# Kernel tuning notes

Hardware: AMD Instinct MI355X
Metric: run time of the kernel (lower is better)

## Reference

```python
import jax, jax.numpy as jnp
import numpy as np
import math

EMB = 64
NEG_INF = -1e30

def _layernorm(x, g, b, eps=1e-5):
    mu = jnp.mean(x, axis=-1, keepdims=True)
    var = jnp.mean((x - mu) ** 2, axis=-1, keepdims=True)
    return (x - mu) * jax.lax.rsqrt(var + eps) * g + b

def setup_inputs() -> dict:
    key = jax.random.key(0)
    ks = jax.random.split(key, 8)
    b, t, n, d = 16, 12, 307, EMB
    s = 1.0 / math.sqrt(d)
    inp = {
        'x': jax.random.normal(ks[0], (b, t, n, d), dtype=jnp.float32),
        'stg': jax.random.uniform(ks[1], (b, n, t, n), dtype=jnp.float32),
        'topk': 3,
        'q_w': jax.random.normal(ks[2], (d, d), dtype=jnp.float32) * s,
        'q_b': jnp.zeros((d,), jnp.float32),
        'k_w': jax.random.normal(ks[3], (d, d), dtype=jnp.float32) * s,
        'k_b': jnp.zeros((d,), jnp.float32),
        'ln_g': jnp.ones((d,), jnp.float32),
        'ln_b': jnp.zeros((d,), jnp.float32),
        'ffn_ln_g': jnp.ones((d,), jnp.float32),
        'ffn_ln_b': jnp.zeros((d,), jnp.float32),
        'fc1_w': jax.random.normal(ks[4], (4 * d, d), dtype=jnp.float32) * s,
        'fc1_b': jnp.zeros((4 * d,), jnp.float32),
        'fc2_w': jax.random.normal(ks[5], (d, 4 * d), dtype=jnp.float32) * (0.5 * s),
        'fc2_b': jnp.zeros((d,), jnp.float32),
    }
    return inp

def reference(x, stg, topk, q_w, q_b, k_w, k_b, ln_g, ln_b, ffn_ln_g, ffn_ln_b, fc1_w, fc1_b, fc2_w, fc2_b):
    b, t, n, d = x.shape
    scale = 1.0 / math.sqrt(d)
    x_ = _layernorm(x, ln_g, ln_b)           # [b,t,n,d]
    y_ = x_[:, -1]                            # [b,n,d] last timestep
    q = y_ @ q_w.T + q_b                      # [b,n,d]
    k = x_ @ k_w.T + k_b                      # [b,t,n,d]
    dg = jnp.einsum('bnd,btmd->bntm', q, k) * scale
    sag = jax.nn.sigmoid(dg) * stg * scale    # gated scores [b,n,t,n]
    sag = sag.reshape(b, n, t * n)
    if topk > 0:
        kk = topk * n if topk < 5 else topk   # mirrors torch's self.topk *= n
        top_values, _ = jax.lax.top_k(sag, kk)
        thr = top_values[..., -1:]
        sag = jnp.where(sag > thr, sag, NEG_INF)  # strict >, as in torch code
    sag = jax.nn.softmax(sag, axis=-1).reshape(b, n, t, n)  # dropout in eval mode = identity
    o = jnp.einsum('bntm,btmd->bnd', sag, x_)
    h = o + y_
    # FFN: pre-norm residual MLP (LayerNorm -> Linear(d,4d) -> ReLU -> Linear(4d,d) + residual)
    z = _layernorm(h, ffn_ln_g, ffn_ln_b)
    z = jax.nn.relu(z @ fc1_w.T + fc1_b) @ fc2_w.T + fc2_b
    return h + z
```

## Files before the change

kernel.cpp:

```cpp
#include <hip/hip_runtime.h>

typedef __bf16 bf16x8 __attribute__((ext_vector_type(8)));
typedef float  f32x4  __attribute__((ext_vector_type(4)));
typedef unsigned short u16x8 __attribute__((ext_vector_type(8)));
typedef unsigned short u16x4 __attribute__((ext_vector_type(4)));

constexpr int BB    = 16;
constexpr int TT    = 12;
constexpr int NN    = 307;
constexpr int TN    = TT * NN;
constexpr int ROWSX = BB * TT * NN;
constexpr int ROWSH = BB * NN;
constexpr int SST1  = 3712;
constexpr int SSTR  = 3840;
constexpr int HPS   = ROWSH * 64;
constexpr int KQ    = 928;
constexpr float SCALE = 0.125f;

__device__ __forceinline__ float wred_sum(float v) {
#pragma unroll
    for (int m = 32; m > 0; m >>= 1) v += __shfl_xor(v, m, 64);
    return v;
}

__global__ void fold_k(const float* __restrict__ qw, const float* __restrict__ qb,
                       const float* __restrict__ kw, const float* __restrict__ kb,
                       float* __restrict__ M, float* __restrict__ b2,
                       float* __restrict__ vv, float* __restrict__ cc) {
    int e = blockIdx.x, d = threadIdx.x;
    float acc = 0.f;
    for (int dp = 0; dp < 64; ++dp) acc += qw[dp * 64 + e] * kw[dp * 64 + d];
    M[e * 64 + d] = acc;
    float vp = wred_sum(qw[d * 64 + e] * kb[d]);
    if (d == 0) vv[e] = vp;
    if (e == 0) {
        float b = 0.f;
        for (int dp = 0; dp < 64; ++dp) b += qb[dp] * kw[dp * 64 + d];
        b2[d] = b;
        float cp = wred_sum(qb[d] * kb[d]);
        if (d == 0) *cc = cp;
    }
}

__global__ void wconv_k(const float* __restrict__ fc1w, const float* __restrict__ fc2w,
                        __bf16* __restrict__ fc1b16, __bf16* __restrict__ fc2b16) {
    int i = blockIdx.x * 256 + threadIdx.x;
    if (i < 16384) fc1b16[i] = (__bf16)fc1w[i];
    else fc2b16[i - 16384] = (__bf16)fc2w[i - 16384];
}

__global__ __launch_bounds__(256) void lnt_k(const float* __restrict__ x,
                                             const float* __restrict__ g,
                                             const float* __restrict__ b,
                                             __bf16* __restrict__ xnb,
                                             __bf16* __restrict__ xnT,
                                             float* __restrict__ y32) {
    __shared__ unsigned short tile[64][65];
    int bb = blockIdx.y, j0 = blockIdx.x * 64, t = threadIdx.x;
    int w = t >> 6, lane = t & 63;
    float gg = g[lane], bbv = b[lane];
    unsigned short* dst = (unsigned short*)xnT;
#pragma unroll 4
    for (int i = 0; i < 16; ++i) {
        int jr = w * 16 + i;
        int j = j0 + jr;
        bool valid = (j < TN);
        float val = valid ? x[((size_t)bb * TN + j) * 64 + lane] : 0.f;
        float mu  = wred_sum(val) * (1.f / 64.f);
        float dv  = val - mu;
        float var = wred_sum(dv * dv) * (1.f / 64.f);
        float xv  = dv * rsqrtf(var + 1e-5f) * gg + bbv;
        if (valid) {
            __bf16 xb = (__bf16)xv;
            xnb[((size_t)bb * TN + j) * 64 + lane] = xb;
            tile[jr][lane] = *(unsigned short*)&xb;
            if (j >= 11 * NN) y32[((size_t)bb * NN + (j - 11 * NN)) * 64 + lane] = xv;
        } else {
            tile[jr][lane] = 0;
        }
    }
    __syncthreads();
#pragma unroll
    for (int i = 0; i < 16; ++i) {
        int f = t + 256 * i, d = f >> 6, jj = f & 63;
        dst[((size_t)bb * 64 + d) * SSTR + j0 + jj] = tile[jj][d];
    }
}

__global__ __launch_bounds__(256) void qt_k(const float* __restrict__ y32,
                                            const float* __restrict__ M,
                                            const float* __restrict__ b2,
                                            const float* __restrict__ vv,
                                            const float* __restrict__ ccp,
                                            __bf16* __restrict__ qtb,
                                            float* __restrict__ cq) {
    int w = threadIdx.x >> 6, l = threadIdx.x & 63;
    int rr = blockIdx.x * 4 + w;
    if (rr >= ROWSH) return;
    float y = y32[rr * 64 + l];
    float acc = b2[l];
#pragma unroll
    for (int e = 0; e < 64; ++e) acc += __shfl(y, e, 64) * M[e * 64 + l];
    qtb[(size_t)rr * 64 + l] = (__bf16)acc;
    float cp = wred_sum(y * vv[l]);
    if (l == 0) cq[rr] = cp + *ccp;
}

__global__ __launch_bounds__(256) void score_k(const __bf16* __restrict__ qtb,
                                               const float* __restrict__ cq,
                                               const __bf16* __restrict__ xnb,
                                               const float* __restrict__ stg,
                                               __bf16* __restrict__ sag) {
    __shared__ unsigned short wb[64 * 144];
    int bb = blockIdx.z, n0 = blockIdx.y * 64, j0 = blockIdx.x * 128;
    int t = threadIdx.x;
    int w = t >> 6, lane = t & 63;
    int m16 = lane & 15, q4 = lane >> 4;

    bf16x8 a[2][2];
#pragma unroll
    for (int jj = 0; jj < 2; ++jj) {
        const bf16x8* ap = (const bf16x8*)(xnb + ((size_t)bb * TN + j0 + (w * 2 + jj) * 16 + m16) * 64);
        a[jj][0] = ap[q4];
        a[jj][1] = ap[q4 + 4];
    }

    f32x4 acc[2][4];
#pragma unroll
    for (int nt = 0; nt < 4; ++nt) {
        const bf16x8* bp = (const bf16x8*)(qtb + ((size_t)bb * NN + n0 + nt * 16 + m16) * 64);
        bf16x8 b0 = bp[q4], b1 = bp[q4 + 4];
#pragma unroll
        for (int jj = 0; jj < 2; ++jj) {
            f32x4 c = {0.f, 0.f, 0.f, 0.f};
            c = __builtin_amdgcn_mfma_f32_16x16x32_bf16(a[jj][0], b0, c, 0, 0, 0);
            c = __builtin_amdgcn_mfma_f32_16x16x32_bf16(a[jj][1], b1, c, 0, 0, 0);
            acc[jj][nt] = c;
        }
    }

    const float* stgb = stg + (size_t)bb * NN * TN;
#pragma unroll
    for (int nt = 0; nt < 4; ++nt) {
        int n = n0 + nt * 16 + m16;
        float cnv = (n < NN) ? cq[bb * NN + n] : 0.f;
        const float* srow = stgb + (size_t)min(n, NN - 1) * TN;
#pragma unroll
        for (int jj = 0; jj < 2; ++jj) {
            int jb = j0 + (w * 2 + jj) * 16 + q4 * 4;
            float4 sv = {0.f, 0.f, 0.f, 0.f};
            if (jb < TN) sv = *(const float4*)(srow + jb);
            u16x4 hw;
            float svv[4] = {sv.x, sv.y, sv.z, sv.w};
#pragma unroll
            for (int r = 0; r < 4; ++r) {
                float dg = (acc[jj][nt][r] + cnv) * SCALE;
                float s  = 1.f / (1.f + __expf(-dg));
                float wv = (jb + r < TN) ? s * svv[r] * SCALE : 0.f;
                __bf16 wb16 = (__bf16)wv;
                hw[r] = *(unsigned short*)&wb16;
            }
            *(u16x4*)&wb[(nt * 16 + m16) * 144 + (w * 2 + jj) * 16 + q4 * 4] = hw;
        }
    }
    __syncthreads();

#pragma unroll
    for (int i = 0; i < 4; ++i) {
        int chunk = t + i * 256;
        int row = chunk >> 4, c8 = (chunk & 15) * 8;
        int n = n0 + row;
        if (n < NN) {
            u16x8 v = *(const u16x8*)&wb[row * 144 + c8];
            *(u16x8*)((unsigned short*)sag + (size_t)(bb * NN + n) * SST1 + j0 + c8) = v;
        }
    }
}

__global__ __launch_bounds__(256) void smax_k(__bf16* __restrict__ sagB,
                                              const int* __restrict__ topk_p,
                                              float* __restrict__ rsum) {
    int t = threadIdx.x;
    int wid = t >> 6, lane = t & 63;
    int row = blockIdx.x * 4 + wid;
    if (row >= ROWSH) return;

    int topkv = *topk_p;
    bool selAll = (topkv <= 0);
    int kk = 0;
    if (!selAll) {
        kk = (topkv < 5) ? topkv * NN : topkv;
        if (kk > TN) kk = TN;
    }

    u16x8* src = (u16x8*)((unsigned short*)sagB + (size_t)row * SST1);
    u16x8 va[8];
#pragma unroll
    for (int ci = 0; ci < 8; ++ci) {
        int c = lane + (ci << 6);
        u16x8 v = {0, 0, 0, 0, 0, 0, 0, 0};
        if (c < 464) v = src[c];
        va[ci] = v;
    }
    int vmb = 0;
#pragma unroll
    for (int ci = 0; ci < 8; ++ci)
#pragma unroll
        for (int e = 0; e < 8; ++e) vmb = max(vmb, (int)va[ci][e]);
#pragma unroll
    for (int m = 32; m > 0; m >>= 1) vmb = max(vmb, __shfl_xor(vmb, m, 64));
    float vmax = __uint_as_float(((unsigned)vmb) << 16);

    unsigned thrb = 0;
    if (!selAll) {
        unsigned lo = 0, hi = (unsigned)vmb;
        while (lo < hi) {
            unsigned mid = (lo + hi) >> 1;
            int cnt = 0;
#pragma unroll
            for (int ci = 0; ci < 8; ++ci)
#pragma unroll
                for (int e = 0; e < 8; ++e)
                    cnt += (int)__popcll(__ballot((unsigned)va[ci][e] > mid));
            if (cnt < kk) hi = mid; else lo = mid + 1;
        }
        thrb = lo;
    }

    float local = 0.f;
#pragma unroll
    for (int ci = 0; ci < 8; ++ci) {
        int c = lane + (ci << 6);
        int nvv = (c < 460) ? 8 : ((c == 460) ? 4 : 0);
#pragma unroll
        for (int e = 0; e < 8; ++e) {
            unsigned u = va[ci][e];
            bool sel = selAll ? (e < nvv) : (u > thrb);
            float ev = sel ? __expf(__uint_as_float(u << 16) - vmax) : 0.f;
            local += ev;
            __bf16 eb = (__bf16)ev;
            va[ci][e] = *(unsigned short*)&eb;
        }
    }
    local = wred_sum(local);
    bool uni = !(local > 0.f);
    if (lane == 0) rsum[row] = uni ? (float)TN : local;

    if (uni) {
        __bf16 one = (__bf16)1.f, zero = (__bf16)0.f;
#pragma unroll
        for (int ci = 0; ci < 8; ++ci) {
            int c = lane + (ci << 6);
            if (c < 464) {
                int nvv = (c < 460) ? 8 : ((c == 460) ? 4 : 0);
                bf16x8 o;
#pragma unroll
                for (int e = 0; e < 8; ++e) o[e] = (e < nvv) ? one : zero;
                *(bf16x8*)&src[c] = o;
            }
        }
    } else {
#pragma unroll
        for (int ci = 0; ci < 8; ++ci) {
            int c = lane + (ci << 6);
            if (c < 464) src[c] = va[ci];
        }
    }
}

__global__ __launch_bounds__(256) void pv_k(const __bf16* __restrict__ sagB,
                                            const __bf16* __restrict__ xnT,
                                            const float* __restrict__ y32,
                                            const float* __restrict__ rsum,
                                            float* __restrict__ hp) {
    int bb = blockIdx.z, kq = blockIdx.y, n0 = blockIdx.x * 16;
    int wid = threadIdx.x >> 6, lane = threadIdx.x & 63;
    int m16 = lane & 15, q4 = lane >> 4;

    int arow = min(n0 + m16, NN - 1);
    const __bf16* ab  = sagB + (size_t)(bb * NN + arow) * SST1 + kq * KQ + q4 * 8;
    const __bf16* bbp = xnT + ((size_t)bb * 64 + wid * 16 + m16) * SSTR + kq * KQ + q4 * 8;

    f32x4 acc0 = {0.f, 0.f, 0.f, 0.f}, acc1 = {0.f, 0.f, 0.f, 0.f};
#pragma unroll 4
    for (int ks = 0; ks < 29; ++ks) {
        bf16x8 a = *(const bf16x8*)(ab + ks * 32);
        bf16x8 b = *(const bf16x8*)(bbp + ks * 32);
        if (ks & 1) acc1 = __builtin_amdgcn_mfma_f32_16x16x32_bf16(a, b, acc1, 0, 0, 0);
        else        acc0 = __builtin_amdgcn_mfma_f32_16x16x32_bf16(a, b, acc0, 0, 0, 0);
    }
#pragma unroll
    for (int r = 0; r < 4; ++r) {
        int n = n0 + q4 * 4 + r;
        if (n < NN) {
            size_t o = (size_t)(bb * NN + n) * 64 + wid * 16 + m16;
            float inv = 1.f / rsum[bb * NN + n];
            float v = (acc0[r] + acc1[r]) * inv;
            if (kq == 0) v += y32[o];
            hp[(size_t)kq * HPS + o] = v;
        }
    }
}

__global__ __launch_bounds__(256) void ffn_k(const float* __restrict__ hp,
                                             const float* __restrict__ g,
                                             const float* __restrict__ bln,
                                             const __bf16* __restrict__ fc1b16,
                                             const float* __restrict__ fc1b,
                                             const __bf16* __restrict__ fc2b16,
                                             const float* __restrict__ fc2b,
                                             float* __restrict__ out) {
    __shared__ __bf16 zb[16 * 68];
    __shared__ __bf16 ab[16 * 264];
    int t = threadIdx.x, r0 = blockIdx.x * 16;
    int wid = t >> 6, lane = t & 63;
    int m16 = lane & 15, q4 = lane >> 4;

#pragma unroll
    for (int q = 0; q < 4; ++q) {
        int rl = wid * 4 + q;
        size_t i = (size_t)(r0 + rl) * 64 + lane;
        float val = hp[i] + hp[HPS + i] + hp[2 * HPS + i] + hp[3 * HPS + i];
        float mu  = wred_sum(val) * (1.f / 64.f);
        float dv  = val - mu;
        float var = wred_sum(dv * dv) * (1.f / 64.f);
        zb[rl * 68 + lane] = (__bf16)(dv * rsqrtf(var + 1e-5f) * g[lane] + bln[lane]);
    }
    __syncthreads();

    bf16x8 a0 = *(const bf16x8*)&zb[m16 * 68 + q4 * 8];
    bf16x8 a1 = *(const bf16x8*)&zb[m16 * 68 + 32 + q4 * 8];
#pragma unroll
    for (int jt2 = 0; jt2 < 4; ++jt2) {
        int j0t = (wid * 4 + jt2) * 16;
        const __bf16* bp = fc1b16 + (size_t)(j0t + m16) * 64 + q4 * 8;
        f32x4 c = {0.f, 0.f, 0.f, 0.f};
        c = __builtin_amdgcn_mfma_f32_16x16x32_bf16(a0, *(const bf16x8*)bp, c, 0, 0, 0);
        c = __builtin_amdgcn_mfma_f32_16x16x32_bf16(a1, *(const bf16x8*)(bp + 32), c, 0, 0, 0);
        int j = j0t + m16;
        float bias = fc1b[j];
#pragma unroll
        for (int r = 0; r < 4; ++r)
            ab[(q4 * 4 + r) * 264 + j] = (__bf16)fmaxf(c[r] + bias, 0.f);
    }
    __syncthreads();

    f32x4 c2a = {0.f, 0.f, 0.f, 0.f}, c2b = {0.f, 0.f, 0.f, 0.f};
    const __bf16* b2p = fc2b16 + (size_t)(wid * 16 + m16) * 256 + q4 * 8;
#pragma unroll
    for (int k8 = 0; k8 < 8; k8 += 2) {
        bf16x8 aa0 = *(const bf16x8*)&ab[m16 * 264 + k8 * 32 + q4 * 8];
        bf16x8 aa1 = *(const bf16x8*)&ab[m16 * 264 + (k8 + 1) * 32 + q4 * 8];
        c2a = __builtin_amdgcn_mfma_f32_16x16x32_bf16(aa0, *(const bf16x8*)(b2p + k8 * 32), c2a, 0, 0, 0);
        c2b = __builtin_amdgcn_mfma_f32_16x16x32_bf16(aa1, *(const bf16x8*)(b2p + (k8 + 1) * 32), c2b, 0, 0, 0);
    }
    int d = wid * 16 + m16;
    float bias2 = fc2b[d];
#pragma unroll
    for (int r = 0; r < 4; ++r) {
        size_t row = (size_t)(r0 + q4 * 4 + r);
        size_t o = row * 64 + d;
        float hsum = hp[o] + hp[HPS + o] + hp[2 * HPS + o] + hp[3 * HPS + o];
        out[o] = hsum + c2a[r] + c2b[r] + bias2;
    }
}

extern "C" void kernel_launch(void* const* d_in, const int* in_sizes, int n_in,
                              void* d_out, int out_size, void* d_ws, size_t ws_size,
                              hipStream_t stream) {
    const float* x    = (const float*)d_in[0];
    const float* stg  = (const float*)d_in[1];
    const int*   topk = (const int*)d_in[2];
    const float* qw   = (const float*)d_in[3];
    const float* qb   = (const float*)d_in[4];
    const float* kw   = (const float*)d_in[5];
    const float* kb   = (const float*)d_in[6];
    const float* lng  = (const float*)d_in[7];
    const float* lnb  = (const float*)d_in[8];
    const float* flng = (const float*)d_in[9];
    const float* flnb = (const float*)d_in[10];
    const float* fc1w = (const float*)d_in[11];
    const float* fc1b = (const float*)d_in[12];
    const float* fc2w = (const float*)d_in[13];
    const float* fc2b = (const float*)d_in[14];
    float* out = (float*)d_out;

    float* ws = (float*)d_ws;
    __bf16* xnb = (__bf16*)ws;
    float* p1   = ws + 1886208;
    __bf16* xnT = (__bf16*)p1;
    float* p2   = p1 + 1966080;
    __bf16* qtb = (__bf16*)p2;
    float* y32  = p2 + 157696;
    float* cq   = y32 + 314368;
    float* M    = cq + 4928;
    float* b2   = M + 4096;
    float* vv   = b2 + 64;
    float* cc   = vv + 64;
    __bf16* fc1b16 = (__bf16*)(cc + 16);
    __bf16* fc2b16 = (__bf16*)((float*)fc1b16 + 8192);
    __bf16* sag = (__bf16*)((float*)fc2b16 + 8192);
    float* hp   = (float*)sag + 9116672;
    float* rsum = hp + 4 * HPS;

    fold_k<<<64, 64, 0, stream>>>(qw, qb, kw, kb, M, b2, vv, cc);
    wconv_k<<<128, 256, 0, stream>>>(fc1w, fc2w, fc1b16, fc2b16);
    lnt_k<<<dim3(58, BB), 256, 0, stream>>>(x, lng, lnb, xnb, xnT, y32);
    qt_k<<<(ROWSH + 3) / 4, 256, 0, stream>>>(y32, M, b2, vv, cc, qtb, cq);
    score_k<<<dim3((TN + 127) / 128, (NN + 63) / 64, BB), 256, 0, stream>>>(qtb, cq, xnb, stg, sag);
    smax_k<<<(ROWSH + 3) / 4, 256, 0, stream>>>(sag, topk, rsum);
    pv_k<<<dim3((NN + 15) / 16, 4, BB), 256, 0, stream>>>(sag, xnT, y32, rsum, hp);
    ffn_k<<<ROWSH / 16, 256, 0, stream>>>(hp, flng, flnb, fc1b16, fc1b, fc2b16, fc2b, out);
}
```

Before: 266.4 us.

## Split layernorm and transpose into separate kernels; prefetch stg loads in score kernel

The fused layernorm-plus-transpose kernel becomes two kernels. One does a row-parallel layernorm with one wave per row across many more blocks. The other transposes the bf16 normalized data through shared memory. In the score kernel the stg gate values and cq loads are issued before the MFMA work to hide global latency, launch bounds request 4 blocks per CU, and the LDS row stride changes from 144 to 152. The split adds a kernel launch and an extra read of xnb in exchange for more parallelism in the layernorm.

After: 256.5 us. -3.7%, faster.

```diff
diff --git a/kernel.cpp b/kernel.cpp
--- a/kernel.cpp
+++ b/kernel.cpp
@@ -15,6 +15,7 @@
 constexpr int SSTR  = 3840;
 constexpr int HPS   = ROWSH * 64;
 constexpr int KQ    = 928;
+constexpr int WBS   = 152;
 constexpr float SCALE = 0.125f;
 
 __device__ __forceinline__ float wred_sum(float v) {
@@ -49,35 +50,38 @@
     else fc2b16[i - 16384] = (__bf16)fc2w[i - 16384];
 }
 
-__global__ __launch_bounds__(256) void lnt_k(const float* __restrict__ x,
-                                             const float* __restrict__ g,
-                                             const float* __restrict__ b,
-                                             __bf16* __restrict__ xnb,
-                                             __bf16* __restrict__ xnT,
-                                             float* __restrict__ y32) {
+__global__ __launch_bounds__(256) void ln_k(const float* __restrict__ x,
+                                            const float* __restrict__ g,
+                                            const float* __restrict__ b,
+                                            __bf16* __restrict__ xnb,
+                                            float* __restrict__ y32) {
+    int w = threadIdx.x >> 6, l = threadIdx.x & 63;
+    int r = blockIdx.x * 4 + w;
+    if (r >= ROWSX) return;
+    float val = x[r * 64 + l];
+    float mu  = wred_sum(val) * (1.f / 64.f);
+    float dv  = val - mu;
+    float var = wred_sum(dv * dv) * (1.f / 64.f);
+    float xv  = dv * rsqrtf(var + 1e-5f) * g[l] + b[l];
+    xnb[(size_t)r * 64 + l] = (__bf16)xv;
+    int t = (r / NN) % TT;
+    if (t == TT - 1) {
+        int bbv = r / (NN * TT), n = r % NN;
+        y32[(bbv * NN + n) * 64 + l] = xv;
+    }
+}
+
+__global__ __launch_bounds__(256) void t_k(const __bf16* __restrict__ xnb,
+                                           __bf16* __restrict__ xnT) {
     __shared__ unsigned short tile[64][65];
     int bb = blockIdx.y, j0 = blockIdx.x * 64, t = threadIdx.x;
-    int w = t >> 6, lane = t & 63;
-    float gg = g[lane], bbv = b[lane];
+    const unsigned short* src = (const unsigned short*)xnb;
     unsigned short* dst = (unsigned short*)xnT;
-#pragma unroll 4
+#pragma unroll
     for (int i = 0; i < 16; ++i) {
-        int jr = w * 16 + i;
+        int f = t + 256 * i, jr = f >> 6, dc = f & 63;
         int j = j0 + jr;
-        bool valid = (j < TN);
-        float val = valid ? x[((size_t)bb * TN + j) * 64 + lane] : 0.f;
-        float mu  = wred_sum(val) * (1.f / 64.f);
-        float dv  = val - mu;
-        float var = wred_sum(dv * dv) * (1.f / 64.f);
-        float xv  = dv * rsqrtf(var + 1e-5f) * gg + bbv;
-        if (valid) {
-            __bf16 xb = (__bf16)xv;
-            xnb[((size_t)bb * TN + j) * 64 + lane] = xb;
-            tile[jr][lane] = *(unsigned short*)&xb;
-            if (j >= 11 * NN) y32[((size_t)bb * NN + (j - 11 * NN)) * 64 + lane] = xv;
-        } else {
-            tile[jr][lane] = 0;
-        }
+        tile[jr][dc] = (j < TN) ? src[((size_t)bb * TN + j) * 64 + dc] : (unsigned short)0;
     }
     __syncthreads();
 #pragma unroll
@@ -106,16 +110,39 @@
     if (l == 0) cq[rr] = cp + *ccp;
 }
 
-__global__ __launch_bounds__(256) void score_k(const __bf16* __restrict__ qtb,
-                                               const float* __restrict__ cq,
-                                               const __bf16* __restrict__ xnb,
-                                               const float* __restrict__ stg,
-                                               __bf16* __restrict__ sag) {
-    __shared__ unsigned short wb[64 * 144];
+__global__ __launch_bounds__(256, 4) void score_k(const __bf16* __restrict__ qtb,
+                                                  const float* __restrict__ cq,
+                                                  const __bf16* __restrict__ xnb,
+                                                  const float* __restrict__ stg,
+                                                  __bf16* __restrict__ sag) {
+    __shared__ unsigned short wb[64 * WBS];
     int bb = blockIdx.z, n0 = blockIdx.y * 64, j0 = blockIdx.x * 128;
     int t = threadIdx.x;
     int w = t >> 6, lane = t & 63;
     int m16 = lane & 15, q4 = lane >> 4;
+
+    const float* stgb = stg + (size_t)bb * NN * TN;
+    float4 sv[4][2];
+    float cn[4];
+#pragma unroll
+    for (int nt = 0; nt < 4; ++nt) {
+        int n = n0 + nt * 16 + m16;
+        const float* srow = stgb + (size_t)min(n, NN - 1) * TN;
+#pragma unroll
+        for (int jj = 0; jj < 2; ++jj) {
+            int jb = j0 + (w * 2 + jj) * 16 + q4 * 4;
+            float4 s4 = {0.f, 0.f, 0.f, 0.f};
+            if (jb < TN) s4 = *(const float4*)(srow + jb);
+            sv[nt][jj] = s4;
+        }
+        int nc = n0 + nt * 16 + m16;
+        cn[nt] = 0.f;
+    }
+#pragma unroll
+    for (int nt = 0; nt < 4; ++nt) {
+        int n = n0 + nt * 16 + m16;
+        cn[nt] = (n < NN) ? cq[bb * NN + n] : 0.f;
+    }
 
     bf16x8 a[2][2];
 #pragma unroll
@@ -139,28 +166,22 @@
         }
     }
 
-    const float* stgb = stg + (size_t)bb * NN * TN;
 #pragma unroll
     for (int nt = 0; nt < 4; ++nt) {
-        int n = n0 + nt * 16 + m16;
-        float cnv = (n < NN) ? cq[bb * NN + n] : 0.f;
-        const float* srow = stgb + (size_t)min(n, NN - 1) * TN;
 #pragma unroll
         for (int jj = 0; jj < 2; ++jj) {
             int jb = j0 + (w * 2 + jj) * 16 + q4 * 4;
-            float4 sv = {0.f, 0.f, 0.f, 0.f};
-            if (jb < TN) sv = *(const float4*)(srow + jb);
+            float svv[4] = {sv[nt][jj].x, sv[nt][jj].y, sv[nt][jj].z, sv[nt][jj].w};
             u16x4 hw;
-            float svv[4] = {sv.x, sv.y, sv.z, sv.w};
 #pragma unroll
             for (int r = 0; r < 4; ++r) {
-                float dg = (acc[jj][nt][r] + cnv) * SCALE;
+                float dg = (acc[jj][nt][r] + cn[nt]) * SCALE;
                 float s  = 1.f / (1.f + __expf(-dg));
                 float wv = (jb + r < TN) ? s * svv[r] * SCALE : 0.f;
                 __bf16 wb16 = (__bf16)wv;
                 hw[r] = *(unsigned short*)&wb16;
             }
-            *(u16x4*)&wb[(nt * 16 + m16) * 144 + (w * 2 + jj) * 16 + q4 * 4] = hw;
+            *(u16x4*)&wb[(nt * 16 + m16) * WBS + (w * 2 + jj) * 16 + q4 * 4] = hw;
         }
     }
     __syncthreads();
@@ -171,7 +192,7 @@
         int row = chunk >> 4, c8 = (chunk & 15) * 8;
         int n = n0 + row;
         if (n < NN) {
-            u16x8 v = *(const u16x8*)&wb[row * 144 + c8];
+            u16x8 v = *(const u16x8*)&wb[row * WBS + c8];
             *(u16x8*)((unsigned short*)sag + (size_t)(bb * NN + n) * SST1 + j0 + c8) = v;
         }
     }
@@ -405,7 +426,8 @@
 
     fold_k<<<64, 64, 0, stream>>>(qw, qb, kw, kb, M, b2, vv, cc);
     wconv_k<<<128, 256, 0, stream>>>(fc1w, fc2w, fc1b16, fc2b16);
-    lnt_k<<<dim3(58, BB), 256, 0, stream>>>(x, lng, lnb, xnb, xnT, y32);
+    ln_k<<<(ROWSX + 3) / 4, 256, 0, stream>>>(x, lng, lnb, xnb, y32);
+    t_k<<<dim3((TN + 63) / 64, BB), 256, 0, stream>>>(xnb, xnT);
     qt_k<<<(ROWSH + 3) / 4, 256, 0, stream>>>(y32, M, b2, vv, cc, qtb, cq);
     score_k<<<dim3((TN + 127) / 128, (NN + 63) / 64, BB), 256, 0, stream>>>(qtb, cq, xnb, stg, sag);
     smax_k<<<(ROWSH + 3) / 4, 256, 0, stream>>>(sag, topk, rsum);
```
